# Performance work log

Hardware: AMD Instinct MI355X
Metric: run time of the kernel (lower is better)

Reference implementation:

```python
import jax, jax.numpy as jnp
import numpy as np

N = 262144
H = 128            # hidden_features
NB = 8             # hidden_layers
CD = 128           # c_dim // 2
ENC_P = 3 * 2 * 10 + 3   # 63
ENC_V = 3 * 2 * 4 + 3    # 27


def encode_points(p, L):
    # concat [p, sin(2^i p), cos(2^i p)] for i in 0..L-1, matching torch concat order
    freqs = 2.0 ** jnp.arange(L, dtype=p.dtype)            # [L]
    ang = p[..., None, :] * freqs[:, None]                 # [..., L, 3]
    sc = jnp.concatenate([jnp.sin(ang), jnp.cos(ang)], axis=-1)  # [..., L, 6]
    sc = sc.reshape(*p.shape[:-1], L * 2 * p.shape[-1])
    return jnp.concatenate([p, sc], axis=-1)


def setup_inputs() -> dict:
    key = jax.random.key(0)
    ks = jax.random.split(key, 24)
    s = 0.05
    inp = {
        "coords": (jax.random.uniform(ks[0], (N, 3)) * 2.0 - 1.0) * 3.0,  # in (-pi, pi)
        "condition": jax.random.normal(ks[1], (N, 2 * CD)),
        "ray_dir": jax.random.normal(ks[2], (N, 3)),
        "noise": jax.random.normal(ks[3], (N, 1)),
        "W_in": jax.random.normal(ks[4], (ENC_P, H)) * s, "b_in": jnp.zeros((H,)),
        "W_blocks": jax.random.normal(ks[5], (NB, H, H)) * s, "b_blocks": jnp.zeros((NB, H)),
        "W_c": jax.random.normal(ks[6], (CD, H)) * s, "b_c": jnp.zeros((H,)),
        "W_skip": jax.random.normal(ks[7], (ENC_P, H)) * s, "b_skip": jnp.zeros((H,)),
        "W_skipc": jax.random.normal(ks[8], (CD, H)) * s, "b_skipc": jnp.zeros((H,)),
        "W_out": jax.random.normal(ks[9], (H, 1)) * s, "b_out": jnp.zeros((1,)),
        "W_viewc": jax.random.normal(ks[10], (CD, H)) * s, "b_viewc": jnp.zeros((H,)),
        "W_view": jax.random.normal(ks[11], (ENC_V, H)) * s, "b_view": jnp.zeros((H,)),
        "W_rgb": jax.random.normal(ks[12], (H, 3)) * s, "b_rgb": jnp.zeros((3,)),
    }
    return inp


def reference(coords, condition, ray_dir, noise,
              W_in, b_in, W_blocks, b_blocks, W_c, b_c,
              W_skip, b_skip, W_skipc, b_skipc, W_out, b_out,
              W_viewc, b_viewc, W_view, b_view, W_rgb, b_rgb):
    relu = jax.nn.relu
    cond_shape, cond_app = condition[..., :CD], condition[..., CD:]
    enc = encode_points(coords, 10)                       # [N, 63]
    net = enc @ W_in + b_in + (cond_shape @ W_c + b_c)
    for idx in range(NB):
        if idx == 4:  # skips=[4]
            net = net + (enc @ W_skip + b_skip) + (cond_shape @ W_skipc + b_skipc)
        net = relu(net) @ W_blocks[idx] + b_blocks[idx]
    sigma = relu(net) @ W_out + b_out                     # density_offset = 0
    sigma = sigma + noise * 1.0                           # raw_noise_std = 1.0
    sigma = relu(sigma)                                   # activate_sigma
    rd = ray_dir / jnp.linalg.norm(ray_dir, axis=-1, keepdims=True)
    enc_v = encode_points(rd, 4)                          # [N, 27]
    net = net + (enc_v @ W_view + b_view) + (cond_app @ W_viewc + b_viewc)
    rgb = jax.nn.sigmoid(relu(net) @ W_rgb + b_rgb)       # net_view: ReLU -> Linear(128,3)
    return jnp.concatenate([sigma, rgb], axis=-1)
```

## Files before the change

kernel.cpp:

```cpp
#include <hip/hip_runtime.h>
#include <hip/hip_bf16.h>

typedef unsigned int u32;
typedef unsigned short u16;

using bf16x8 = __attribute__((ext_vector_type(8))) short;
using f32x4  = __attribute__((ext_vector_type(4))) float;

#define OFF_IN     0L
#define OFF_C      18432L
#define OFF_B0     53248L
#define OFF_SKIP   331776L
#define OFF_SKIPC  350208L
#define OFF_VIEW   385024L
#define OFF_VIEWC  395264L
#define OFF_BIAS0  430080L
#define OFF_BIASSK 430592L
#define OFF_BIASV  431104L

#define LDS_X   0
#define LDS_W   34816
#define LDS_SP  69632
#define LDS_RP  70656
#define LDS_TOTAL 73728

__device__ __forceinline__ u16 f2bf(float x) {
  union { float f; u32 u; } un; un.f = x;
  u32 u = un.u;
  return (u16)((u + 0x7fffu + ((u >> 16) & 1u)) >> 16);
}
__device__ __forceinline__ u32 pack2(float a, float b) {
  u32 r;
  asm("v_cvt_pk_bf16_f32 %0, %1, %2" : "=v"(r) : "v"(a), "v"(b));
  return r;
}
__device__ __forceinline__ float sel3(float a, float b, float c, int i) {
  return i == 0 ? a : (i == 1 ? b : c);
}
__device__ __forceinline__ float enc_val3(float a, float b, float c, int e, int kreal) {
  if (e >= kreal) return 0.f;
  if (e < 3) return sel3(a, b, c, e);
  int t = e - 3;
  int l = t / 6;
  int rem = t - l * 6;
  int pi = rem >= 3 ? rem - 3 : rem;
  float x = sel3(a, b, c, pi) * (float)(1 << l);
  return rem < 3 ? __sinf(x) : __cosf(x);
}
__device__ __forceinline__ bf16x8 mk8(u32 a, u32 b, u32 c, u32 d) {
  union { u32 u[4]; bf16x8 v; } t; t.u[0] = a; t.u[1] = b; t.u[2] = c; t.u[3] = d;
  return t.v;
}
__device__ __forceinline__ void gll16(const void* g, void* l) {
  __builtin_amdgcn_global_load_lds(
      (const __attribute__((address_space(1))) void*)g,
      (__attribute__((address_space(3))) void*)l, 16, 0, 0);
}

__global__ void prep_kernel(
    const float* __restrict__ Win, const float* __restrict__ Wc, const float* __restrict__ Wb,
    const float* __restrict__ Wskip, const float* __restrict__ Wskipc,
    const float* __restrict__ Wview, const float* __restrict__ Wviewc,
    const float* __restrict__ bin, const float* __restrict__ bc,
    const float* __restrict__ bskip, const float* __restrict__ bskipc,
    const float* __restrict__ bview, const float* __restrict__ bviewc,
    char* __restrict__ ws) {
  int i = blockIdx.x * 256 + threadIdx.x;
  if (i >= 215424) return;
  int r = i;
  const float* src; int kpad, kreal; long dstoff;
  if (r < 9216)                    { src = Win;    kpad = 72;  kreal = 63;  dstoff = OFF_IN; }
  else if ((r -= 9216) < 17408)    { src = Wc;     kpad = 136; kreal = 128; dstoff = OFF_C; }
  else if ((r -= 17408) < 139264)  { int b = r / 17408; r -= b * 17408;
                                     src = Wb + (long)b * 16384; kpad = 136; kreal = 128;
                                     dstoff = OFF_B0 + (long)b * 34816; }
  else if ((r -= 139264) < 9216)   { src = Wskip;  kpad = 72;  kreal = 63;  dstoff = OFF_SKIP; }
  else if ((r -= 9216) < 17408)    { src = Wskipc; kpad = 136; kreal = 128; dstoff = OFF_SKIPC; }
  else if ((r -= 17408) < 5120)    { src = Wview;  kpad = 40;  kreal = 27;  dstoff = OFF_VIEW; }
  else if ((r -= 5120) < 17408)    { src = Wviewc; kpad = 136; kreal = 128; dstoff = OFF_VIEWC; }
  else {
    r -= 17408;
    int which = r >> 7, n = r & 127;
    const float* A  = which == 0 ? bin : (which == 1 ? bskip : bview);
    const float* Bp = which == 0 ? bc  : (which == 1 ? bskipc : bviewc);
    long off = which == 0 ? OFF_BIAS0 : (which == 1 ? OFF_BIASSK : OFF_BIASV);
    *(float*)(ws + off + (long)n * 4) = A[n] + Bp[n];
    return;
  }
  int n = r / kpad, k = r - n * kpad;
  float v = (k < kreal) ? src[(long)k * 128 + n] : 0.f;
  *(u16*)(ws + dstoff + ((long)n * kpad + k) * 2) = f2bf(v);
}

#define GLL_W(off, bytes)                                                      \
  do {                                                                         \
    _Pragma("unroll") for (int it_ = 0; it_ < 9; ++it_) {                      \
      int o_ = it_ * 4096 + wv * 1024;                                         \
      if (o_ < (bytes))                                                        \
        gll16(ws + (off) + o_ + lane * 16, lds + LDS_W + o_);                  \
    }                                                                          \
  } while (0)

#define STREAM_COND(halfsel)                                                   \
  do {                                                                         \
    _Pragma("unroll") for (int c_ = 0; c_ < 4; ++c_) {                         \
      f32x4 v_[4];                                                             \
      _Pragma("unroll") for (int i2 = 0; i2 < 4; ++i2) {                       \
        int f4i = (4 * c_ + i2) * 256 + tid;                                   \
        int row = f4i >> 5, c4 = f4i & 31;                                     \
        v_[i2] = *(const f32x4*)(condition + (size_t)(p0 + row) * 256 +        \
                                 ((halfsel) * 32 + c4) * 4);                   \
      }                                                                        \
      _Pragma("unroll") for (int i2 = 0; i2 < 4; ++i2) {                       \
        int f4i = (4 * c_ + i2) * 256 + tid;                                   \
        int row = f4i >> 5, c4 = f4i & 31;                                     \
        uint2 t_; t_.x = pack2(v_[i2][0], v_[i2][1]);                          \
        t_.y = pack2(v_[i2][2], v_[i2][3]);                                    \
        *(uint2*)(lds + LDS_X + row * 272 + c4 * 8) = t_;                      \
      }                                                                        \
    }                                                                          \
  } while (0)

#define ENC_LOAD_COMPUTE(EF, LAUNDER)                                          \
  do {                                                                         \
    _Pragma("unroll") for (int mi_ = 0; mi_ < 4; ++mi_) {                      \
      int idx_ = p0 + 64 * wr + 16 * mi_ + li;                                 \
      if (LAUNDER) asm volatile("" : "+v"(idx_));                              \
      const float* cp_ = coords + (size_t)idx_ * 3;                            \
      float c0_ = cp_[0], c1_ = cp_[1], c2_ = cp_[2];                          \
      _Pragma("unroll") for (int kt_ = 0; kt_ < 2; ++kt_) {                    \
        u32 w_[4];                                                             \
        _Pragma("unroll") for (int e2_ = 0; e2_ < 4; ++e2_) {                  \
          int k0_ = kt_ * 32 + h * 8 + e2_ * 2;                                \
          w_[e2_] = pack2(enc_val3(c0_, c1_, c2_, k0_, 63),                    \
                          enc_val3(c0_, c1_, c2_, k0_ + 1, 63));               \
        }                                                                      \
        EF[mi_][kt_] = mk8(w_[0], w_[1], w_[2], w_[3]);                        \
      }                                                                        \
    }                                                                          \
  } while (0)

#define GEMM_X(WBASE, NKT)                                                     \
  do {                                                                         \
    _Pragma("unroll") for (int kt = 0; kt < (NKT); ++kt) {                     \
      bf16x8 xf[4];                                                            \
      _Pragma("unroll") for (int mi = 0; mi < 4; ++mi)                         \
        xf[mi] = *(const bf16x8*)(lds + LDS_X + (64*wr + 16*mi + li) * 272 + kt * 64 + h16); \
      _Pragma("unroll") for (int j = 0; j < 4; ++j) {                          \
        bf16x8 wf = *(const bf16x8*)(lds + (WBASE) + (64*wc + 16*j + li) * 272 + kt * 64 + h16); \
        _Pragma("unroll") for (int mi = 0; mi < 4; ++mi)                       \
          acc[mi][j] = __builtin_amdgcn_mfma_f32_16x16x32_bf16(wf, xf[mi], acc[mi][j], 0, 0, 0); \
      }                                                                        \
    }                                                                          \
  } while (0)

#define GEMM_E(WBASE, WSTR, NKT, EF)                                           \
  do {                                                                         \
    _Pragma("unroll") for (int kt = 0; kt < (NKT); ++kt) {                     \
      _Pragma("unroll") for (int j = 0; j < 4; ++j) {                          \
        bf16x8 wf = *(const bf16x8*)(lds + (WBASE) + (64*wc + 16*j + li) * (WSTR) + kt * 64 + h16); \
        _Pragma("unroll") for (int mi = 0; mi < 4; ++mi)                       \
          acc[mi][j] = __builtin_amdgcn_mfma_f32_16x16x32_bf16(wf, (EF)[mi][kt], acc[mi][j], 0, 0, 0); \
      }                                                                        \
    }                                                                          \
  } while (0)

#define ACC_SET(bptr)                                                          \
  do {                                                                         \
    _Pragma("unroll") for (int j = 0; j < 4; ++j) {                            \
      f32x4 b4_ = *(const f32x4*)((bptr) + 64*wc + 16*j + 4*h);                \
      _Pragma("unroll") for (int mi = 0; mi < 4; ++mi) acc[mi][j] = b4_;       \
    }                                                                          \
  } while (0)

#define ACC_ADD(bptr)                                                          \
  do {                                                                         \
    _Pragma("unroll") for (int j = 0; j < 4; ++j) {                            \
      f32x4 b4_ = *(const f32x4*)((bptr) + 64*wc + 16*j + 4*h);                \
      _Pragma("unroll") for (int mi = 0; mi < 4; ++mi) acc[mi][j] += b4_;      \
    }                                                                          \
  } while (0)

#define STORE_X()                                                              \
  do {                                                                         \
    _Pragma("unroll") for (int mi = 0; mi < 4; ++mi)                           \
    _Pragma("unroll") for (int j = 0; j < 4; ++j) {                            \
      f32x4 v_ = acc[mi][j];                                                   \
      uint2 t_;                                                                \
      t_.x = pack2(fmaxf(v_[0], 0.f), fmaxf(v_[1], 0.f));                      \
      t_.y = pack2(fmaxf(v_[2], 0.f), fmaxf(v_[3], 0.f));                      \
      *(uint2*)(lds + LDS_X + (64*wr + 16*mi + li) * 272 + (64*wc + 16*j + 4*h) * 2) = t_; \
    }                                                                          \
  } while (0)

__global__ void __launch_bounds__(256, 2) nerf_main(
    const float* __restrict__ coords, const float* __restrict__ condition,
    const float* __restrict__ ray_dir, const float* __restrict__ noise,
    const float* __restrict__ b_blocks, const float* __restrict__ W_out,
    const float* __restrict__ b_out, const float* __restrict__ W_rgb,
    const float* __restrict__ b_rgb, const char* __restrict__ ws,
    float* __restrict__ out) {
  extern __shared__ __align__(16) char lds[];
  const int tid = threadIdx.x;
  const int lane = tid & 63;
  const int wv = tid >> 6;
  const int wr = wv >> 1, wc = wv & 1;
  const int li = lane & 15, h = lane >> 4;
  const int h16 = h * 16;
  const int p0 = blockIdx.x * 128;

  f32x4 acc[4][4];

  STREAM_COND(0);
  GLL_W(OFF_IN, 18432);
  __syncthreads();

  {
    bf16x8 encf[4][2];
    ENC_LOAD_COMPUTE(encf, 0);
    ACC_SET((const float*)(ws + OFF_BIAS0));
    GEMM_E(LDS_W, 144, 2, encf);
  }
  __syncthreads();
  GLL_W(OFF_C, 34816);
  __syncthreads();

  GEMM_X(LDS_W, 4);
  __syncthreads();
  GLL_W(OFF_B0 + 0L * 34816, 34816);
  STORE_X();
  __syncthreads();

#pragma unroll
  for (int idx = 0; idx < 3; ++idx) {
    ACC_SET(b_blocks + idx * 128);
    GEMM_X(LDS_W, 4);
    __syncthreads();
    GLL_W(OFF_B0 + (idx + 1) * 34816L, 34816);
    STORE_X();
    __syncthreads();
  }

  ACC_SET(b_blocks + 3 * 128);
  GEMM_X(LDS_W, 4);
  __syncthreads();
  GLL_W(OFF_SKIP, 18432);
  STREAM_COND(0);
  __syncthreads();

  {
    bf16x8 encf[4][2];
    ENC_LOAD_COMPUTE(encf, 1);
    ACC_ADD((const float*)(ws + OFF_BIASSK));
    GEMM_E(LDS_W, 144, 2, encf);
  }
  __syncthreads();
  GLL_W(OFF_SKIPC, 34816);
  __syncthreads();

  GEMM_X(LDS_W, 4);
  __syncthreads();
  GLL_W(OFF_B0 + 4L * 34816, 34816);
  STORE_X();
  __syncthreads();

#pragma unroll
  for (int idx = 4; idx < 7; ++idx) {
    ACC_SET(b_blocks + idx * 128);
    GEMM_X(LDS_W, 4);
    __syncthreads();
    GLL_W(OFF_B0 + (idx + 1) * 34816L, 34816);
    STORE_X();
    __syncthreads();
  }

  ACC_SET(b_blocks + 7 * 128);
  GEMM_X(LDS_W, 4);
  float nz = 0.f;
  if (tid < 128) nz = noise[p0 + tid];
  {
    f32x4 wo[4];
#pragma unroll
    for (int j = 0; j < 4; ++j) wo[j] = *(const f32x4*)(W_out + 64 * wc + 16 * j + 4 * h);
#pragma unroll
    for (int mi = 0; mi < 4; ++mi) {
      float s = 0.f;
#pragma unroll
      for (int j = 0; j < 4; ++j)
#pragma unroll
        for (int rr = 0; rr < 4; ++rr) s += fmaxf(acc[mi][j][rr], 0.f) * wo[j][rr];
      s += __shfl_xor(s, 16); s += __shfl_xor(s, 32);
      if (h == 0) *(float*)(lds + LDS_SP + ((64 * wr + 16 * mi + li) * 2 + wc) * 4) = s;
    }
  }
  __syncthreads();
  GLL_W(OFF_VIEW, 10240);
  STREAM_COND(1);
  __syncthreads();

  {
    bf16x8 envf[4][1];
#pragma unroll
    for (int mi = 0; mi < 4; ++mi) {
      size_t base = (size_t)(p0 + 64 * wr + 16 * mi + li) * 3;
      float r0 = ray_dir[base], r1 = ray_dir[base + 1], r2 = ray_dir[base + 2];
      float inv = 1.f / sqrtf(r0 * r0 + r1 * r1 + r2 * r2);
      r0 *= inv; r1 *= inv; r2 *= inv;
      u32 w[4];
#pragma unroll
      for (int e2 = 0; e2 < 4; ++e2) {
        int k0 = h * 8 + e2 * 2;
        w[e2] = pack2(enc_val3(r0, r1, r2, k0, 27), enc_val3(r0, r1, r2, k0 + 1, 27));
      }
      envf[mi][0] = mk8(w[0], w[1], w[2], w[3]);
    }
    ACC_ADD((const float*)(ws + OFF_BIASV));
    GEMM_E(LDS_W, 80, 1, envf);
  }
  float sig = 0.f;
  if (tid < 128) {
    const float* sp = (const float*)(lds + LDS_SP);
    float s = sp[2 * tid] + sp[2 * tid + 1] + b_out[0] + nz;
    sig = fmaxf(s, 0.f);
  }
  __syncthreads();
  GLL_W(OFF_VIEWC, 34816);
  __syncthreads();

  GEMM_X(LDS_W, 4);
  {
#pragma unroll
    for (int mi = 0; mi < 4; ++mi) {
      float s0 = 0.f, s1 = 0.f, s2 = 0.f;
#pragma unroll
      for (int j = 0; j < 4; ++j)
#pragma unroll
        for (int rr = 0; rr < 4; ++rr) {
          float v = fmaxf(acc[mi][j][rr], 0.f);
          int n = 64 * wc + 16 * j + 4 * h + rr;
          s0 += v * W_rgb[n * 3 + 0];
          s1 += v * W_rgb[n * 3 + 1];
          s2 += v * W_rgb[n * 3 + 2];
        }
      s0 += __shfl_xor(s0, 16); s0 += __shfl_xor(s0, 32);
      s1 += __shfl_xor(s1, 16); s1 += __shfl_xor(s1, 32);
      s2 += __shfl_xor(s2, 16); s2 += __shfl_xor(s2, 32);
      if (h == 0) {
        float* rp = (float*)(lds + LDS_RP);
        int m_ = 64 * wr + 16 * mi + li;
        rp[(m_ * 2 + wc) * 3 + 0] = s0;
        rp[(m_ * 2 + wc) * 3 + 1] = s1;
        rp[(m_ * 2 + wc) * 3 + 2] = s2;
      }
    }
  }
  __syncthreads();
  if (tid < 128) {
    const float* rp = (const float*)(lds + LDS_RP);
    f32x4 o4;
    o4[0] = sig;
#pragma unroll
    for (int c = 0; c < 3; ++c) {
      float v = rp[(2 * tid) * 3 + c] + rp[(2 * tid + 1) * 3 + c] + b_rgb[c];
      o4[1 + c] = 1.f / (1.f + __expf(-v));
    }
    *(f32x4*)(out + (size_t)(p0 + tid) * 4) = o4;
  }
}

extern "C" void kernel_launch(void* const* d_in, const int* in_sizes, int n_in,
                              void* d_out, int out_size, void* d_ws, size_t ws_size,
                              hipStream_t stream) {
  const float* coords    = (const float*)d_in[0];
  const float* condition = (const float*)d_in[1];
  const float* ray_dir   = (const float*)d_in[2];
  const float* noise     = (const float*)d_in[3];
  const float* W_in      = (const float*)d_in[4];
  const float* b_in      = (const float*)d_in[5];
  const float* W_blocks  = (const float*)d_in[6];
  const float* b_blocks  = (const float*)d_in[7];
  const float* W_c       = (const float*)d_in[8];
  const float* b_c       = (const float*)d_in[9];
  const float* W_skip    = (const float*)d_in[10];
  const float* b_skip    = (const float*)d_in[11];
  const float* W_skipc   = (const float*)d_in[12];
  const float* b_skipc   = (const float*)d_in[13];
  const float* W_out     = (const float*)d_in[14];
  const float* b_out     = (const float*)d_in[15];
  const float* W_viewc   = (const float*)d_in[16];
  const float* b_viewc   = (const float*)d_in[17];
  const float* W_view    = (const float*)d_in[18];
  const float* b_view    = (const float*)d_in[19];
  const float* W_rgb     = (const float*)d_in[20];
  const float* b_rgb     = (const float*)d_in[21];
  char* ws = (char*)d_ws;
  float* out = (float*)d_out;

  prep_kernel<<<842, 256, 0, stream>>>(W_in, W_c, W_blocks, W_skip, W_skipc, W_view, W_viewc,
                                       b_in, b_c, b_skip, b_skipc, b_view, b_viewc, ws);
  nerf_main<<<2048, 256, LDS_TOTAL, stream>>>(coords, condition, ray_dir, noise,
                                              b_blocks, W_out, b_out, W_rgb, b_rgb, ws, out);
}
```

Measured before the change: 197.5 us.

## Split hidden-layer weights into two K-halves and double-buffer loads across GEMM halves

Each 128x128 hidden weight matrix is now stored as two K-halves (padded first half, XOR-swizzled second half) in separate LDS slots. The load of the next layer's first half is issued while the current layer's second half computes, and vmcnt waits replace full syncthreads, so weight loading overlaps the MFMA work. Biases are staged once into LDS instead of being summed in the prep kernel or read from global memory per layer, and the ray_dir loads are hoisted ahead of a barrier. This adds manual waitcnt/barrier choreography that must stay correct, and LDS use grows to about 79 KB per block, which still allows two blocks per CU.

```diff
diff --git a/kernel.cpp b/kernel.cpp
--- a/kernel.cpp
+++ b/kernel.cpp
@@ -7,22 +7,19 @@
 using bf16x8 = __attribute__((ext_vector_type(8))) short;
 using f32x4  = __attribute__((ext_vector_type(4))) float;
 
-#define OFF_IN     0L
-#define OFF_C      18432L
-#define OFF_B0     53248L
-#define OFF_SKIP   331776L
-#define OFF_SKIPC  350208L
-#define OFF_VIEW   385024L
-#define OFF_VIEWC  395264L
-#define OFF_BIAS0  430080L
-#define OFF_BIASSK 430592L
-#define OFF_BIASV  431104L
+#define OFF_IN    0L
+#define OFF_SKIP  18432L
+#define OFF_VIEW  36864L
+#define HOFF(i)   (47104L + (long)(i) * 34816L)
 
 #define LDS_X   0
-#define LDS_W   34816
+#define LDS_S0  34816
+#define LDS_S1  53248
 #define LDS_SP  69632
 #define LDS_RP  70656
-#define LDS_TOTAL 73728
+#define LDS_B   73728
+#define LDS_TOTAL 79360
+#define BB(i)   (1536 + (i) * 512)
 
 __device__ __forceinline__ u16 f2bf(float x) {
   union { float f; u32 u; } un; un.f = x;
@@ -56,48 +53,55 @@
       (const __attribute__((address_space(1))) void*)g,
       (__attribute__((address_space(3))) void*)l, 16, 0, 0);
 }
+#define MFMA __builtin_amdgcn_mfma_f32_16x16x32_bf16
+#define SBAR __builtin_amdgcn_s_barrier
+#define SCHED0() __builtin_amdgcn_sched_barrier(0)
 
 __global__ void prep_kernel(
     const float* __restrict__ Win, const float* __restrict__ Wc, const float* __restrict__ Wb,
     const float* __restrict__ Wskip, const float* __restrict__ Wskipc,
     const float* __restrict__ Wview, const float* __restrict__ Wviewc,
-    const float* __restrict__ bin, const float* __restrict__ bc,
-    const float* __restrict__ bskip, const float* __restrict__ bskipc,
-    const float* __restrict__ bview, const float* __restrict__ bviewc,
     char* __restrict__ ws) {
   int i = blockIdx.x * 256 + threadIdx.x;
-  if (i >= 215424) return;
+  if (i >= 215040) return;
   int r = i;
-  const float* src; int kpad, kreal; long dstoff;
-  if (r < 9216)                    { src = Win;    kpad = 72;  kreal = 63;  dstoff = OFF_IN; }
-  else if ((r -= 9216) < 17408)    { src = Wc;     kpad = 136; kreal = 128; dstoff = OFF_C; }
-  else if ((r -= 17408) < 139264)  { int b = r / 17408; r -= b * 17408;
-                                     src = Wb + (long)b * 16384; kpad = 136; kreal = 128;
-                                     dstoff = OFF_B0 + (long)b * 34816; }
-  else if ((r -= 139264) < 9216)   { src = Wskip;  kpad = 72;  kreal = 63;  dstoff = OFF_SKIP; }
-  else if ((r -= 9216) < 17408)    { src = Wskipc; kpad = 136; kreal = 128; dstoff = OFF_SKIPC; }
-  else if ((r -= 17408) < 5120)    { src = Wview;  kpad = 40;  kreal = 27;  dstoff = OFF_VIEW; }
-  else if ((r -= 5120) < 17408)    { src = Wviewc; kpad = 136; kreal = 128; dstoff = OFF_VIEWC; }
-  else {
-    r -= 17408;
-    int which = r >> 7, n = r & 127;
-    const float* A  = which == 0 ? bin : (which == 1 ? bskip : bview);
-    const float* Bp = which == 0 ? bc  : (which == 1 ? bskipc : bviewc);
-    long off = which == 0 ? OFF_BIAS0 : (which == 1 ? OFF_BIASSK : OFF_BIASV);
-    *(float*)(ws + off + (long)n * 4) = A[n] + Bp[n];
-    return;
-  }
-  int n = r / kpad, k = r - n * kpad;
-  float v = (k < kreal) ? src[(long)k * 128 + n] : 0.f;
-  *(u16*)(ws + dstoff + ((long)n * kpad + k) * 2) = f2bf(v);
-}
-
-#define GLL_W(off, bytes)                                                      \
-  do {                                                                         \
-    _Pragma("unroll") for (int it_ = 0; it_ < 9; ++it_) {                      \
+  const float* src; long dst; int kreal;
+  if (r < 9216)                  { src = Win;   kreal = 63;
+    int n = r / 72, c = r % 72;
+    float v = (c < 64 && c < kreal) ? src[(long)c * 128 + n] : 0.f;
+    *(u16*)(ws + OFF_IN + ((long)n * 72 + c) * 2) = f2bf(v); return; }
+  else if ((r -= 9216) < 9216)   { src = Wskip; kreal = 63;
+    int n = r / 72, c = r % 72;
+    float v = (c < 64 && c < kreal) ? src[(long)c * 128 + n] : 0.f;
+    *(u16*)(ws + OFF_SKIP + ((long)n * 72 + c) * 2) = f2bf(v); return; }
+  else if ((r -= 9216) < 5120)   { src = Wview; kreal = 27;
+    int n = r / 40, c = r % 40;
+    float v = (c < kreal) ? src[(long)c * 128 + n] : 0.f;
+    *(u16*)(ws + OFF_VIEW + ((long)n * 40 + c) * 2) = f2bf(v); return; }
+  r -= 5120;
+  int hi = r / 17408; r %= 17408;
+  src = hi == 0 ? Wc : hi <= 4 ? Wb + (long)(hi - 1) * 16384
+      : hi == 5 ? Wskipc : hi <= 9 ? Wb + (long)(hi - 2) * 16384 : Wviewc;
+  long hbase = HOFF(hi);
+  if (r < 9216) {
+    int n = r / 72, c = r % 72;
+    float v = (c < 64) ? src[(long)c * 128 + n] : 0.f;
+    *(u16*)(ws + hbase + ((long)n * 72 + c) * 2) = f2bf(v);
+  } else {
+    r -= 9216;
+    int n = r / 64, c = r % 64;
+    float v = src[(long)(64 + c) * 128 + n];
+    long boff = (long)n * 128 + ((c * 2) ^ ((n & 7) << 4));
+    *(u16*)(ws + hbase + 18432 + boff) = f2bf(v);
+  }
+}
+
+#define GLL_CH(woff, lbase, nbytes)                                            \
+  do {                                                                         \
+    _Pragma("unroll") for (int it_ = 0; it_ < 5; ++it_) {                      \
       int o_ = it_ * 4096 + wv * 1024;                                         \
-      if (o_ < (bytes))                                                        \
-        gll16(ws + (off) + o_ + lane * 16, lds + LDS_W + o_);                  \
+      if (o_ < (nbytes))                                                       \
+        gll16(ws + (woff) + o_ + lane * 16, lds + (lbase) + o_);               \
     }                                                                          \
   } while (0)
 
@@ -140,43 +144,80 @@
     }                                                                          \
   } while (0)
 
-#define GEMM_X(WBASE, NKT)                                                     \
-  do {                                                                         \
-    _Pragma("unroll") for (int kt = 0; kt < (NKT); ++kt) {                     \
-      bf16x8 xf[4];                                                            \
-      _Pragma("unroll") for (int mi = 0; mi < 4; ++mi)                         \
-        xf[mi] = *(const bf16x8*)(lds + LDS_X + (64*wr + 16*mi + li) * 272 + kt * 64 + h16); \
-      _Pragma("unroll") for (int j = 0; j < 4; ++j) {                          \
-        bf16x8 wf = *(const bf16x8*)(lds + (WBASE) + (64*wc + 16*j + li) * 272 + kt * 64 + h16); \
-        _Pragma("unroll") for (int mi = 0; mi < 4; ++mi)                       \
-          acc[mi][j] = __builtin_amdgcn_mfma_f32_16x16x32_bf16(wf, xf[mi], acc[mi][j], 0, 0, 0); \
-      }                                                                        \
-    }                                                                          \
-  } while (0)
-
-#define GEMM_E(WBASE, WSTR, NKT, EF)                                           \
-  do {                                                                         \
-    _Pragma("unroll") for (int kt = 0; kt < (NKT); ++kt) {                     \
-      _Pragma("unroll") for (int j = 0; j < 4; ++j) {                          \
-        bf16x8 wf = *(const bf16x8*)(lds + (WBASE) + (64*wc + 16*j + li) * (WSTR) + kt * 64 + h16); \
-        _Pragma("unroll") for (int mi = 0; mi < 4; ++mi)                       \
-          acc[mi][j] = __builtin_amdgcn_mfma_f32_16x16x32_bf16(wf, (EF)[mi][kt], acc[mi][j], 0, 0, 0); \
-      }                                                                        \
-    }                                                                          \
-  } while (0)
-
-#define ACC_SET(bptr)                                                          \
-  do {                                                                         \
+#define GEMM01_BODY(C0EXPR)                                                    \
+  do {                                                                         \
+    bf16x8 xf0[4], xf1[4];                                                     \
+    _Pragma("unroll") for (int mi = 0; mi < 4; ++mi) {                         \
+      const char* xr = lds + LDS_X + (64*wr + 16*mi + li) * 272 + h16;         \
+      xf0[mi] = *(const bf16x8*)(xr);                                          \
+      xf1[mi] = *(const bf16x8*)(xr + 64);                                     \
+    }                                                                          \
     _Pragma("unroll") for (int j = 0; j < 4; ++j) {                            \
-      f32x4 b4_ = *(const f32x4*)((bptr) + 64*wc + 16*j + 4*h);                \
-      _Pragma("unroll") for (int mi = 0; mi < 4; ++mi) acc[mi][j] = b4_;       \
-    }                                                                          \
-  } while (0)
-
-#define ACC_ADD(bptr)                                                          \
-  do {                                                                         \
+      const char* wrp = lds + LDS_S0 + (64*wc + 16*j + li) * 144 + h16;        \
+      bf16x8 wf0 = *(const bf16x8*)(wrp);                                      \
+      bf16x8 wf1 = *(const bf16x8*)(wrp + 64);                                 \
+      _Pragma("unroll") for (int mi = 0; mi < 4; ++mi) {                       \
+        acc[mi][j] = MFMA(wf0, xf0[mi], C0EXPR, 0, 0, 0);                      \
+        acc[mi][j] = MFMA(wf1, xf1[mi], acc[mi][j], 0, 0, 0);                  \
+      }                                                                        \
+    }                                                                          \
+  } while (0)
+
+#define GEMM01_B(BOFF)                                                         \
+  do {                                                                         \
+    f32x4 bias4[4];                                                            \
+    _Pragma("unroll") for (int j = 0; j < 4; ++j)                              \
+      bias4[j] = *(const f32x4*)(lds + LDS_B + (BOFF) + (64*wc + 16*j + 4*h) * 4); \
+    GEMM01_BODY(bias4[j]);                                                     \
+  } while (0)
+#define GEMM01_C() GEMM01_BODY(acc[mi][j])
+
+#define GEMM23()                                                               \
+  do {                                                                         \
+    bf16x8 xf2[4], xf3[4];                                                     \
+    _Pragma("unroll") for (int mi = 0; mi < 4; ++mi) {                         \
+      const char* xr = lds + LDS_X + (64*wr + 16*mi + li) * 272 + 128 + h16;   \
+      xf2[mi] = *(const bf16x8*)(xr);                                          \
+      xf3[mi] = *(const bf16x8*)(xr + 64);                                     \
+    }                                                                          \
+    int swz = (li & 7) << 4;                                                   \
     _Pragma("unroll") for (int j = 0; j < 4; ++j) {                            \
-      f32x4 b4_ = *(const f32x4*)((bptr) + 64*wc + 16*j + 4*h);                \
+      const char* wb = lds + LDS_S1 + (64*wc + 16*j + li) * 128;               \
+      bf16x8 wf2 = *(const bf16x8*)(wb + ((0 + h16) ^ swz));                   \
+      bf16x8 wf3 = *(const bf16x8*)(wb + ((64 + h16) ^ swz));                  \
+      _Pragma("unroll") for (int mi = 0; mi < 4; ++mi) {                       \
+        acc[mi][j] = MFMA(wf2, xf2[mi], acc[mi][j], 0, 0, 0);                  \
+        acc[mi][j] = MFMA(wf3, xf3[mi], acc[mi][j], 0, 0, 0);                  \
+      }                                                                        \
+    }                                                                          \
+  } while (0)
+
+#define GEMME01_BODY(EF, C0EXPR)                                               \
+  do {                                                                         \
+    _Pragma("unroll") for (int j = 0; j < 4; ++j) {                            \
+      const char* wrp = lds + LDS_S0 + (64*wc + 16*j + li) * 144 + h16;        \
+      bf16x8 wf0 = *(const bf16x8*)(wrp);                                      \
+      bf16x8 wf1 = *(const bf16x8*)(wrp + 64);                                 \
+      _Pragma("unroll") for (int mi = 0; mi < 4; ++mi) {                       \
+        acc[mi][j] = MFMA(wf0, EF[mi][0], C0EXPR, 0, 0, 0);                    \
+        acc[mi][j] = MFMA(wf1, EF[mi][1], acc[mi][j], 0, 0, 0);                \
+      }                                                                        \
+    }                                                                          \
+  } while (0)
+
+#define GEMME01_B(BOFF, EF)                                                    \
+  do {                                                                         \
+    f32x4 bias4[4];                                                            \
+    _Pragma("unroll") for (int j = 0; j < 4; ++j)                              \
+      bias4[j] = *(const f32x4*)(lds + LDS_B + (BOFF) + (64*wc + 16*j + 4*h) * 4); \
+    GEMME01_BODY(EF, bias4[j]);                                                \
+  } while (0)
+#define GEMME01_C(EF) GEMME01_BODY(EF, acc[mi][j])
+
+#define ACC_ADD_LDS(BOFF)                                                      \
+  do {                                                                         \
+    _Pragma("unroll") for (int j = 0; j < 4; ++j) {                            \
+      f32x4 b4_ = *(const f32x4*)(lds + LDS_B + (BOFF) + (64*wc + 16*j + 4*h) * 4); \
       _Pragma("unroll") for (int mi = 0; mi < 4; ++mi) acc[mi][j] += b4_;      \
     }                                                                          \
   } while (0)
@@ -193,10 +234,46 @@
     }                                                                          \
   } while (0)
 
+#define PHASE_MID(BOFF, NOFF)                                                  \
+  do {                                                                         \
+    if ((BOFF) >= 0) { GEMM01_B(BOFF); } else { GEMM01_C(); }                  \
+    SBAR();                                      \
+    GLL_CH((NOFF), LDS_S0, 18432);                                             \
+    asm volatile("s_waitcnt vmcnt(4)" ::: "memory");        \
+    SCHED0(); SBAR();                                                          \
+    GEMM23();                                                                  \
+    SBAR();                                               \
+    GLL_CH((NOFF) + 18432, LDS_S1, 16384);                                     \
+    asm volatile("s_waitcnt vmcnt(4)" ::: "memory");       \
+    SCHED0();                                                                  \
+    STORE_X();                                                                 \
+    asm volatile("s_waitcnt lgkmcnt(0)" ::: "memory");                         \
+    SCHED0(); SBAR();                           \
+  } while (0)
+
+#define PHASE_LAST(BOFF)                                                       \
+  do {                                                                         \
+    if ((BOFF) >= 0) { GEMM01_B(BOFF); } else { GEMM01_C(); }                  \
+    asm volatile("s_waitcnt vmcnt(0)" ::: "memory");        \
+    SCHED0(); SBAR();                                                          \
+    GEMM23();                                                                  \
+  } while (0)
+
+#define PRELOAD(NOFF)                                                          \
+  do {                                                                         \
+    GLL_CH((NOFF), LDS_S0, 18432);                                             \
+    GLL_CH((NOFF) + 18432, LDS_S1, 16384);                                     \
+    asm volatile("s_waitcnt vmcnt(4)" ::: "memory");             \
+    SCHED0(); SBAR();                                                          \
+  } while (0)
+
 __global__ void __launch_bounds__(256, 2) nerf_main(
     const float* __restrict__ coords, const float* __restrict__ condition,
     const float* __restrict__ ray_dir, const float* __restrict__ noise,
-    const float* __restrict__ b_blocks, const float* __restrict__ W_out,
+    const float* __restrict__ b_in, const float* __restrict__ b_c,
+    const float* __restrict__ b_blocks, const float* __restrict__ b_skip,
+    const float* __restrict__ b_skipc, const float* __restrict__ b_view,
+    const float* __restrict__ b_viewc, const float* __restrict__ W_out,
     const float* __restrict__ b_out, const float* __restrict__ W_rgb,
     const float* __restrict__ b_rgb, const char* __restrict__ ws,
     float* __restrict__ out) {
@@ -211,73 +288,55 @@
 
   f32x4 acc[4][4];
 
+#pragma unroll
+  for (int it = 0; it < 6; ++it) {
+    int i = tid + it * 256;
+    if (i < 1408) {
+      float v = i < 128 ? b_in[i] + b_c[i]
+              : i < 256 ? b_skip[i - 128] + b_skipc[i - 128]
+              : i < 384 ? b_view[i - 256] + b_viewc[i - 256]
+              : b_blocks[i - 384];
+      *(float*)(lds + LDS_B + (long)i * 4) = v;
+    }
+  }
   STREAM_COND(0);
-  GLL_W(OFF_IN, 18432);
+  GLL_CH(OFF_IN, LDS_S0, 18432);
   __syncthreads();
 
   {
     bf16x8 encf[4][2];
     ENC_LOAD_COMPUTE(encf, 0);
-    ACC_SET((const float*)(ws + OFF_BIAS0));
-    GEMM_E(LDS_W, 144, 2, encf);
-  }
-  __syncthreads();
-  GLL_W(OFF_C, 34816);
-  __syncthreads();
-
-  GEMM_X(LDS_W, 4);
-  __syncthreads();
-  GLL_W(OFF_B0 + 0L * 34816, 34816);
-  STORE_X();
-  __syncthreads();
-
-#pragma unroll
-  for (int idx = 0; idx < 3; ++idx) {
-    ACC_SET(b_blocks + idx * 128);
-    GEMM_X(LDS_W, 4);
-    __syncthreads();
-    GLL_W(OFF_B0 + (idx + 1) * 34816L, 34816);
-    STORE_X();
-    __syncthreads();
-  }
-
-  ACC_SET(b_blocks + 3 * 128);
-  GEMM_X(LDS_W, 4);
-  __syncthreads();
-  GLL_W(OFF_SKIP, 18432);
+    GEMME01_B(0, encf);
+  }
+  __syncthreads();
+
+  PRELOAD(HOFF(0));
+  PHASE_MID(-1, HOFF(1));
+  PHASE_MID(BB(0), HOFF(2));
+  PHASE_MID(BB(1), HOFF(3));
+  PHASE_MID(BB(2), HOFF(4));
+  PHASE_LAST(BB(3));
+
+  GLL_CH(OFF_SKIP, LDS_S0, 18432);
+  __syncthreads();
   STREAM_COND(0);
   __syncthreads();
 
   {
     bf16x8 encf[4][2];
     ENC_LOAD_COMPUTE(encf, 1);
-    ACC_ADD((const float*)(ws + OFF_BIASSK));
-    GEMM_E(LDS_W, 144, 2, encf);
-  }
-  __syncthreads();
-  GLL_W(OFF_SKIPC, 34816);
-  __syncthreads();
-
-  GEMM_X(LDS_W, 4);
-  __syncthreads();
-  GLL_W(OFF_B0 + 4L * 34816, 34816);
-  STORE_X();
-  __syncthreads();
-
-#pragma unroll
-  for (int idx = 4; idx < 7; ++idx) {
-    ACC_SET(b_blocks + idx * 128);
-    GEMM_X(LDS_W, 4);
-    __syncthreads();
-    GLL_W(OFF_B0 + (idx + 1) * 34816L, 34816);
-    STORE_X();
-    __syncthreads();
-  }
-
-  ACC_SET(b_blocks + 7 * 128);
-  GEMM_X(LDS_W, 4);
-  float nz = 0.f;
-  if (tid < 128) nz = noise[p0 + tid];
+    ACC_ADD_LDS(512);
+    GEMME01_C(encf);
+  }
+  __syncthreads();
+
+  PRELOAD(HOFF(5));
+  PHASE_MID(-1, HOFF(6));
+  PHASE_MID(BB(4), HOFF(7));
+  PHASE_MID(BB(5), HOFF(8));
+  PHASE_MID(BB(6), HOFF(9));
+  PHASE_LAST(BB(7));
+
   {
     f32x4 wo[4];
 #pragma unroll
@@ -294,16 +353,29 @@
     }
   }
   __syncthreads();
-  GLL_W(OFF_VIEW, 10240);
+  GLL_CH(OFF_VIEW, LDS_S0, 10240);
   STREAM_COND(1);
-  __syncthreads();
+  float nz = 0.f;
+  if (tid < 128) nz = noise[p0 + tid];
+  float ray0[4], ray1[4], ray2[4];
+#pragma unroll
+  for (int mi = 0; mi < 4; ++mi) {
+    size_t base = (size_t)(p0 + 64 * wr + 16 * mi + li) * 3;
+    ray0[mi] = ray_dir[base]; ray1[mi] = ray_dir[base + 1]; ray2[mi] = ray_dir[base + 2];
+  }
+  __syncthreads();
+  float sig = 0.f;
+  if (tid < 128) {
+    const float* sp = (const float*)(lds + LDS_SP);
+    float s = sp[2 * tid] + sp[2 * tid + 1] + b_out[0] + nz;
+    sig = fmaxf(s, 0.f);
+  }
 
   {
     bf16x8 envf[4][1];
 #pragma unroll
     for (int mi = 0; mi < 4; ++mi) {
-      size_t base = (size_t)(p0 + 64 * wr + 16 * mi + li) * 3;
-      float r0 = ray_dir[base], r1 = ray_dir[base + 1], r2 = ray_dir[base + 2];
+      float r0 = ray0[mi], r1 = ray1[mi], r2 = ray2[mi];
       float inv = 1.f / sqrtf(r0 * r0 + r1 * r1 + r2 * r2);
       r0 *= inv; r1 *= inv; r2 *= inv;
       u32 w[4];
@@ -314,20 +386,20 @@
       }
       envf[mi][0] = mk8(w[0], w[1], w[2], w[3]);
     }
-    ACC_ADD((const float*)(ws + OFF_BIASV));
-    GEMM_E(LDS_W, 80, 1, envf);
-  }
-  float sig = 0.f;
-  if (tid < 128) {
-    const float* sp = (const float*)(lds + LDS_SP);
-    float s = sp[2 * tid] + sp[2 * tid + 1] + b_out[0] + nz;
-    sig = fmaxf(s, 0.f);
-  }
-  __syncthreads();
-  GLL_W(OFF_VIEWC, 34816);
-  __syncthreads();
-
-  GEMM_X(LDS_W, 4);
+    ACC_ADD_LDS(1024);
+#pragma unroll
+    for (int j = 0; j < 4; ++j) {
+      bf16x8 wf = *(const bf16x8*)(lds + LDS_S0 + (64 * wc + 16 * j + li) * 80 + h16);
+#pragma unroll
+      for (int mi = 0; mi < 4; ++mi)
+        acc[mi][j] = MFMA(wf, envf[mi][0], acc[mi][j], 0, 0, 0);
+    }
+  }
+  __syncthreads();
+
+  PRELOAD(HOFF(10));
+  PHASE_LAST(-1);
+
   {
 #pragma unroll
     for (int mi = 0; mi < 4; ++mi) {
@@ -396,8 +468,10 @@
   char* ws = (char*)d_ws;
   float* out = (float*)d_out;
 
-  prep_kernel<<<842, 256, 0, stream>>>(W_in, W_c, W_blocks, W_skip, W_skipc, W_view, W_viewc,
-                                       b_in, b_c, b_skip, b_skipc, b_view, b_viewc, ws);
+  prep_kernel<<<840, 256, 0, stream>>>(W_in, W_c, W_blocks, W_skip, W_skipc,
+                                       W_view, W_viewc, ws);
   nerf_main<<<2048, 256, LDS_TOTAL, stream>>>(coords, condition, ray_dir, noise,
-                                              b_blocks, W_out, b_out, W_rgb, b_rgb, ws, out);
-}
+                                              b_in, b_c, b_blocks, b_skip, b_skipc,
+                                              b_view, b_viewc, W_out, b_out,
+                                              W_rgb, b_rgb, ws, out);
+}
```

Result: no change. 194.6 us (-1.5%).
